# Kernel optimization log

Hardware: AMD Instinct MI355X
Metric: run time of the kernel (lower is better)

Reference implementation:

```python
import jax, jax.numpy as jnp
import numpy as np

# ---- static config (from MACEConfig / MACELayerConfig) ----
N_NODES = 128
F_S = 128          # n_invariant_feat_hidden (0e channels)
F_V = 64           # n_vectors_hidden (1e channels)
N_BESSEL = 8       # bessel_number
R_MAX = 5.0        # r_max
N_LAYERS = 2       # n_interactions
HID_RAD = 64       # radial MLP hidden width
F_S_OUT = 128      # n_invariant_feat_readout
F_V_OUT = 64       # n_vectors_readout
AVG_NEIGH = float(N_NODES)  # avg_num_neighbors default = n_nodes
RAD_OUT = F_S + 3 * F_V     # per-edge radial channel weights for the 4 TP paths


def _senders_receivers(n):
    # fully connected graph, matching get_senders_and_receivers
    s = np.repeat(np.arange(n), n - 1)
    j = np.tile(np.arange(1, n), n)
    r = (s + j) % n
    return jnp.asarray(s, dtype=jnp.int32), jnp.asarray(r, dtype=jnp.int32)


def _bessel(r):
    # e3nn bessel basis: sqrt(2/c) sin(n pi r / c) / r, n = 1..N_BESSEL
    n = jnp.arange(1, N_BESSEL + 1, dtype=r.dtype)
    return jnp.sqrt(2.0 / R_MAX) * jnp.sin(n * jnp.pi * r[:, None] / R_MAX) / r[:, None]


def _envelope(r):
    # smooth radial cutoff (polynomial p=6), stand-in for e3nn soft_envelope
    u = r / R_MAX
    p = 6.0
    env = 1.0 - (p + 1) * (p + 2) / 2 * u ** p + p * (p + 2) * u ** (p + 1) - p * (p + 1) / 2 * u ** (p + 2)
    return jnp.where(u < 1.0, env, 0.0)


def _forward(x, species_embed, Wr1, Wr2, W_sv, W_mix_s, W_mix_v, W_out_s, W_out_v):
    senders, receivers = _senders_receivers(N_NODES)

    def single(pos):  # pos: (N, 3)
        com = pos.mean(axis=0)                       # centre of mass (3,)
        v = pos[receivers] - pos[senders]            # edge relative vectors (E, 3)
        r = jnp.linalg.norm(v, axis=-1) + 1e-8       # (E,)
        vhat = v / r[:, None]
        rb = _bessel(r) * _envelope(r)[:, None]      # (E, N_BESSEL)

        s = jnp.broadcast_to(species_embed[0], (N_NODES, F_S))       # 0e node feats
        V = jnp.zeros((N_NODES, F_V, 3), dtype=pos.dtype)            # 1e node feats

        for l in range(N_LAYERS):
            # learned per-edge radial weights for each tensor-product path
            h = jax.nn.silu(rb @ Wr1[l]) @ Wr2[l]    # (E, RAD_OUT)
            R0 = h[:, :F_S]
            R1 = h[:, F_S:F_S + F_V]
            R2 = h[:, F_S + F_V:F_S + 2 * F_V]
            R3 = h[:, F_S + 2 * F_V:]

            s_src = s[senders]                       # gather (E, F_S)
            V_src = V[senders]                       # gather (E, F_V, 3)

            # CG tensor-product paths (only 0e and 1e irreps present):
            m0a = R0 * s_src                                         # 0e x 0e -> 0e
            m0b = R1 * jnp.einsum('efk,ek->ef', V_src, vhat)         # 1e x 1e -> 0e
            m1a = (R2 * (s_src @ W_sv[l]))[..., None] * vhat[:, None, :]  # 0e x 1e -> 1e
            m1b = R3[..., None] * V_src                              # 1e x 0e -> 1e

            # scatter-sum message passing over receivers
            agg0 = jax.ops.segment_sum(jnp.concatenate([m0a, m0b], -1), receivers,
                                       num_segments=N_NODES) / AVG_NEIGH   # (N, F_S+F_V)
            agg1 = jax.ops.segment_sum(jnp.concatenate([m1a, m1b], 1), receivers,
                                       num_segments=N_NODES) / AVG_NEIGH   # (N, 2F_V, 3)

            s = s + jax.nn.silu(agg0 @ W_mix_s[l])
            V = V + jnp.einsum('nfk,fg->ngk', agg1, W_mix_v[l])

        out_s = s @ W_out_s                                          # (N, F_S_OUT)
        out_v = jnp.einsum('nfk,fg->ngk', V, W_out_v) + com          # (N, F_V_OUT, 3) + CoM
        return out_v, out_s

    return jax.vmap(single)(x)


def setup_inputs() -> dict:
    key = jax.random.key(0)
    ks = jax.random.split(key, 10)
    sc = lambda fan: 1.0 / np.sqrt(fan)
    inp = {
        'x': jax.random.normal(ks[0], (8, N_NODES, 3), dtype=jnp.float32),
        'species_embed': jax.random.normal(ks[1], (1, F_S), dtype=jnp.float32),
        'Wr1': jax.random.normal(ks[2], (N_LAYERS, N_BESSEL, HID_RAD), dtype=jnp.float32) * sc(N_BESSEL),
        'Wr2': jax.random.normal(ks[3], (N_LAYERS, HID_RAD, RAD_OUT), dtype=jnp.float32) * sc(HID_RAD),
        'W_sv': jax.random.normal(ks[4], (N_LAYERS, F_S, F_V), dtype=jnp.float32) * sc(F_S),
        'W_mix_s': jax.random.normal(ks[5], (N_LAYERS, F_S + F_V, F_S), dtype=jnp.float32) * sc(F_S + F_V),
        'W_mix_v': jax.random.normal(ks[6], (N_LAYERS, 2 * F_V, F_V), dtype=jnp.float32) * sc(2 * F_V),
        'W_out_s': jax.random.normal(ks[7], (F_S, F_S_OUT), dtype=jnp.float32) * sc(F_S),
        'W_out_v': jax.random.normal(ks[8], (F_V, F_V_OUT), dtype=jnp.float32) * sc(F_V),
    }
    return inp


def reference(x, species_embed, Wr1, Wr2, W_sv, W_mix_s, W_mix_v, W_out_s, W_out_v):
    return _forward(x, species_embed, Wr1, Wr2, W_sv, W_mix_s, W_mix_v, W_out_s, W_out_v)
```

## Files before the change

### kernel.cpp

```cpp
#include <hip/hip_runtime.h>
#include <math.h>

typedef unsigned short u16;
typedef __attribute__((ext_vector_type(8))) short frag_ab;
typedef __attribute__((ext_vector_type(4))) float frag_cd;

#define BATCH 8
#define NN 128
#define FS 128
#define FV 64
#define NB 8
#define HID 64
#define ROUT 320
#define HSTRB 72

#define SZ_S (BATCH*FS*NN)
#define SZ_V (BATCH*FV*3*NN)
#define SZ_T (BATCH*FV*NN)
#define N_W2B (ROUT*HID)
#define OFF_SB 0
#define OFF_VB (OFF_SB+SZ_S)
#define OFF_T1 (OFF_VB+SZ_V)
#define OFF_W2B (OFF_T1+SZ_T)

__device__ __forceinline__ float silu_f(float x){ return x * (1.0f/(1.0f + __expf(-x))); }

__device__ __forceinline__ u16 f2bf(float x){
  union { float f; unsigned int u; } v; v.f = x;
  unsigned int r = v.u + 0x7fffu + ((v.u >> 16) & 1u);
  return (u16)(r >> 16);
}
__device__ __forceinline__ float bf2f(u16 h){
  union { unsigned int u; float f; } v; v.u = ((unsigned int)h) << 16; return v.f;
}

__global__ __launch_bounds__(512) void layer0_kernel(
    const float* __restrict__ pos,
    const float* __restrict__ species,
    const float* __restrict__ Wr1l,
    const float* __restrict__ Wr2,
    const float* __restrict__ Wsv,
    const float* __restrict__ WmixSl,
    const float* __restrict__ WmixVl,
    float* __restrict__ sOut,
    float* __restrict__ vOut,
    float* __restrict__ tOut,
    u16*   __restrict__ w2b)
{
  const int tid = threadIdx.x;
  const int b   = blockIdx.x >> 6;
  const int k0  = (blockIdx.x & 63) * 2;

  __shared__ u16   hidB[2][128*HSTRB];
  __shared__ float vhx[2][128], vhy[2][128], vhz[2][128];
  __shared__ float colsum[2][4][64];
  __shared__ float aggS[2][128];
  __shared__ float dV[2][192];
  __shared__ float sNew[2][128];
  __shared__ float t0L[64];

  const float* pb   = pos + b*NN*3;
  const float* Wr2l = Wr2;

  {
    const int kk   = tid >> 8;
    const int r2   = tid & 255;
    const int i    = r2 & 127;
    const int half = r2 >> 7;
    const int k    = k0 + kk;
    float vx = pb[k*3+0]-pb[i*3+0];
    float vy = pb[k*3+1]-pb[i*3+1];
    float vz = pb[k*3+2]-pb[i*3+2];
    float r = sqrtf(vx*vx+vy*vy+vz*vz) + 1e-8f;
    float inv = 1.0f/r;
    if (half==0){ vhx[kk][i]=vx*inv; vhy[kk][i]=vy*inv; vhz[kk][i]=vz*inv; }
    float u = r*0.2f;
    float env = 0.0f;
    if (u < 1.0f && i != k){
      float u2=u*u, u6=u2*u2*u2;
      env = 1.0f - 28.0f*u6 + 48.0f*u6*u - 21.0f*u6*u2;
    }
    float coef = 0.6324555320336759f * inv * env;
    float th   = r * 0.6283185307179586f;
    float s1 = __sinf(th), c1 = __cosf(th);
    float rb[NB];
    rb[0] = coef*s1;
    float twoc = 2.f*c1, sp = s1, spp = 0.f;
    #pragma unroll
    for(int n=1;n<NB;n++){ float s = twoc*sp - spp; spp = sp; sp = s; rb[n] = coef*s; }
    u16* hrow = hidB[kk] + i*HSTRB;
    #pragma unroll
    for(int jg=0;jg<8;jg++){
      const int jgg = half*8 + jg;
      float h0=0.f,h1=0.f,h2=0.f,h3=0.f;
      #pragma unroll
      for(int n=0;n<NB;n++){
        const float* wr = Wr1l + n*HID + jgg*4;
        float rn = rb[n];
        h0 = fmaf(rn, wr[0], h0);
        h1 = fmaf(rn, wr[1], h1);
        h2 = fmaf(rn, wr[2], h2);
        h3 = fmaf(rn, wr[3], h3);
      }
      ushort4 uu = make_ushort4(f2bf(silu_f(h0)), f2bf(silu_f(h1)),
                                f2bf(silu_f(h2)), f2bf(silu_f(h3)));
      *(ushort4*)(hrow + jgg*4) = uu;
    }
  }
  __syncthreads();

  {
    const int kk  = tid >> 8;
    const int var = (tid >> 6) & 3;
    const int j   = tid & 63;
    const u16* hb = hidB[kk];
    float a0 = 0.f, a1 = 0.f;
    if (var == 0){
      #pragma unroll 8
      for (int i=0;i<128;i+=2){
        a0 += bf2f(hb[i*HSTRB + j]);
        a1 += bf2f(hb[(i+1)*HSTRB + j]);
      }
    } else {
      const float* wv = (var==1) ? vhx[kk] : (var==2) ? vhy[kk] : vhz[kk];
      #pragma unroll 8
      for (int i=0;i<128;i+=2){
        a0 = fmaf(bf2f(hb[i*HSTRB + j]),     wv[i],   a0);
        a1 = fmaf(bf2f(hb[(i+1)*HSTRB + j]), wv[i+1], a1);
      }
    }
    colsum[kk][var][j] = a0+a1;
  }
  __syncthreads();

  if (tid < 128){
    const int c = tid;
    float d00=0.f,d01=0.f, d10=0.f,d11=0.f;
    #pragma unroll 8
    for (int j=0;j<HID;j+=2){
      float w0 = Wr2l[j*ROUT + c];
      float w1 = Wr2l[(j+1)*ROUT + c];
      d00 = fmaf(colsum[0][0][j],   w0, d00);
      d01 = fmaf(colsum[0][0][j+1], w1, d01);
      d10 = fmaf(colsum[1][0][j],   w0, d10);
      d11 = fmaf(colsum[1][0][j+1], w1, d11);
    }
    float sc = species[c] * (1.0f/128.0f);
    aggS[0][c] = sc * (d00+d01);
    aggS[1][c] = sc * (d10+d11);
  } else if (tid < 320){
    const int o = tid - 128;
    const int f = o & 63, c3 = o >> 6;
    float d00=0.f,d01=0.f, d10=0.f,d11=0.f;
    #pragma unroll 8
    for (int j=0;j<HID;j+=2){
      float w0 = Wr2l[j*ROUT + 192 + f];
      float w1 = Wr2l[(j+1)*ROUT + 192 + f];
      d00 = fmaf(colsum[0][1+c3][j],   w0, d00);
      d01 = fmaf(colsum[0][1+c3][j+1], w1, d01);
      d10 = fmaf(colsum[1][1+c3][j],   w0, d10);
      d11 = fmaf(colsum[1][1+c3][j+1], w1, d11);
    }
    dV[0][f*3+c3] = (d00+d01) * (1.0f/128.0f);
    dV[1][f*3+c3] = (d10+d11) * (1.0f/128.0f);
  } else if (tid < 384){
    const int g = tid - 320;
    float a0=0.f, a1=0.f;
    #pragma unroll 8
    for (int c=0; c<FS; c+=2){
      a0 = fmaf(species[c],   Wsv[c*FV+g],     a0);
      a1 = fmaf(species[c+1], Wsv[(c+1)*FV+g], a1);
    }
    t0L[g] = a0+a1;
  } else if (tid < 424){
    const int t = blockIdx.x*40 + (tid-384);
    const int j = t & 63, c = t >> 6;
    w2b[t] = f2bf(Wr2[HID*ROUT + j*ROUT + c]);
  }
  __syncthreads();

  if (tid < FS){
    float a00=0.f,a01=0.f, a10=0.f,a11=0.f;
    #pragma unroll 8
    for (int cc=0; cc<128; cc+=2){
      float w0 = WmixSl[cc*FS+tid];
      float w1 = WmixSl[(cc+1)*FS+tid];
      a00 = fmaf(aggS[0][cc],   w0, a00);
      a01 = fmaf(aggS[0][cc+1], w1, a01);
      a10 = fmaf(aggS[1][cc],   w0, a10);
      a11 = fmaf(aggS[1][cc+1], w1, a11);
    }
    float sn0 = species[tid] + silu_f(a00+a01);
    float sn1 = species[tid] + silu_f(a10+a11);
    sNew[0][tid] = sn0;
    sNew[1][tid] = sn1;
    sOut[(b*FS+tid)*NN + k0]     = sn0;
    sOut[(b*FS+tid)*NN + k0 + 1] = sn1;
  } else if (tid < 320){
    const int o = tid - 128;
    const int g = o/3, c3 = o - g*3;
    float a0=0.f, a1=0.f;
    #pragma unroll 8
    for (int f=0; f<FV; f++){
      float w = WmixVl[f*FV+g];
      float tf = t0L[f];
      a0 = fmaf(tf*dV[0][f*3+c3], w, a0);
      a1 = fmaf(tf*dV[1][f*3+c3], w, a1);
    }
    vOut[(b*FV*3 + o)*NN + k0]     = a0;
    vOut[(b*FV*3 + o)*NN + k0 + 1] = a1;
  }
  __syncthreads();

  if (tid < FV){
    const float* Wsv1 = Wsv + FS*FV;
    float a00=0.f,a01=0.f, a10=0.f,a11=0.f;
    #pragma unroll 8
    for (int f=0; f<FS; f+=2){
      float w0 = Wsv1[f*FV+tid];
      float w1 = Wsv1[(f+1)*FV+tid];
      a00 = fmaf(sNew[0][f],   w0, a00);
      a01 = fmaf(sNew[0][f+1], w1, a01);
      a10 = fmaf(sNew[1][f],   w0, a10);
      a11 = fmaf(sNew[1][f+1], w1, a11);
    }
    tOut[(b*FV+tid)*NN + k0]     = (a00+a01);
    tOut[(b*FV+tid)*NN + k0 + 1] = (a10+a11);
  }
}

__global__ __launch_bounds__(512) void layer_kernel(
    const float* __restrict__ pos,
    const float* __restrict__ sIn,
    const float* __restrict__ vIn,
    const float* __restrict__ tIn,
    const float* __restrict__ Wr1l,
    const u16*   __restrict__ w2bl,
    const float* __restrict__ WmixSl,
    const float* __restrict__ WmixVl,
    const float* __restrict__ WoutS,
    const float* __restrict__ WoutV,
    float* __restrict__ outp)
{
  const int tid  = threadIdx.x;
  const int b    = blockIdx.x >> 5;
  const int k0   = (blockIdx.x & 31) * 4;
  const int w    = tid >> 6;
  const int lane = tid & 63;
  const int col  = lane & 15;
  const int quad = lane >> 4;
  const int wq   = w & 3;
  const int sh   = w >> 2;

  __shared__ u16   hidB[4][128*HSTRB];
  __shared__ float vhx[4][128], vhy[4][128], vhz[4][128];
  __shared__ float aggP[4][2][576];
  __shared__ float sPart[4][2][FS];
  __shared__ float sNew[4][FS];
  __shared__ float vNewL[4][192];
  __shared__ float comL[3];

  const float* pb = pos + b*NN*3;

  {
    const int kk = tid >> 7;
    const int i  = tid & 127;
    const int k  = k0 + kk;
    float vx = pb[k*3+0]-pb[i*3+0];
    float vy = pb[k*3+1]-pb[i*3+1];
    float vz = pb[k*3+2]-pb[i*3+2];
    float r = sqrtf(vx*vx+vy*vy+vz*vz) + 1e-8f;
    float inv = 1.0f/r;
    vhx[kk][i]=vx*inv; vhy[kk][i]=vy*inv; vhz[kk][i]=vz*inv;
    float u = r*0.2f;
    float env = 0.0f;
    if (u < 1.0f && i != k){
      float u2=u*u, u6=u2*u2*u2;
      env = 1.0f - 28.0f*u6 + 48.0f*u6*u - 21.0f*u6*u2;
    }
    float coef = 0.6324555320336759f * inv * env;
    float th   = r * 0.6283185307179586f;
    float s1 = __sinf(th), c1 = __cosf(th);
    float rb[NB];
    rb[0] = coef*s1;
    float twoc = 2.f*c1, sp = s1, spp = 0.f;
    #pragma unroll
    for(int n=1;n<NB;n++){ float s = twoc*sp - spp; spp = sp; sp = s; rb[n] = coef*s; }
    u16* hrow = hidB[kk] + i*HSTRB;
    #pragma unroll
    for(int jg=0;jg<16;jg++){
      float h0=0.f,h1=0.f,h2=0.f,h3=0.f;
      #pragma unroll
      for(int n=0;n<NB;n++){
        const float* wr = Wr1l + n*HID + jg*4;
        float rn = rb[n];
        h0 = fmaf(rn, wr[0], h0);
        h1 = fmaf(rn, wr[1], h1);
        h2 = fmaf(rn, wr[2], h2);
        h3 = fmaf(rn, wr[3], h3);
      }
      ushort4 uu = make_ushort4(f2bf(silu_f(h0)), f2bf(silu_f(h1)),
                                f2bf(silu_f(h2)), f2bf(silu_f(h3)));
      *(ushort4*)(hrow + jg*4) = uu;
    }
    if (tid < 3){
      float a0=0.f, a1=0.f;
      for (int n=0;n<NN;n+=2){ a0 += pb[n*3+tid]; a1 += pb[(n+1)*3+tid]; }
      comL[tid] = (a0+a1) * (1.0f/128.0f);
    }
  }
  __syncthreads();

  const float* sIb = sIn + b*FS*NN;
  const float* vIb = vIn + b*FV*3*NN;
  const float* tIb = tIn + b*FV*NN;
  const int i00 = sh*64 + quad*4;

  {
    const int c_s0 = wq*16 + col;
    const int c_s1 = 64 + c_s0;
    const int f_vc = c_s0;

    const u16* wp0 = w2bl + c_s0*HID + quad*8;
    const u16* wp1 = w2bl + c_s1*HID + quad*8;
    const u16* wp2 = w2bl + (128 + f_vc)*HID + quad*8;
    const u16* wp3 = w2bl + (192 + f_vc)*HID + quad*8;
    const u16* wp4 = w2bl + (256 + f_vc)*HID + quad*8;
    const frag_ab b00 = *(const frag_ab*)(wp0), b01 = *(const frag_ab*)(wp0+32);
    const frag_ab b10 = *(const frag_ab*)(wp1), b11 = *(const frag_ab*)(wp1+32);
    const frag_ab b20 = *(const frag_ab*)(wp2), b21 = *(const frag_ab*)(wp2+32);
    const frag_ab b30 = *(const frag_ab*)(wp3), b31 = *(const frag_ab*)(wp3+32);
    const frag_ab b40 = *(const frag_ab*)(wp4), b41 = *(const frag_ab*)(wp4+32);

    const float* fs0 = sIb + c_s0*NN + i00;
    const float* fs1 = sIb + c_s1*NN + i00;
    const float* fv  = vIb + f_vc*3*NN + i00;
    const float* ft  = tIb + f_vc*NN + i00;

    float sA0[4]={0.f,0.f,0.f,0.f}, sA1[4]={0.f,0.f,0.f,0.f}, sA2[4]={0.f,0.f,0.f,0.f};
    float sX3[4]={0.f,0.f,0.f,0.f}, sY3[4]={0.f,0.f,0.f,0.f}, sZ3[4]={0.f,0.f,0.f,0.f};
    float sX4[4]={0.f,0.f,0.f,0.f}, sY4[4]={0.f,0.f,0.f,0.f}, sZ4[4]={0.f,0.f,0.f,0.f};

    #pragma unroll 1
    for (int mt=0; mt<4; mt++){
      float4 s4a = *(const float4*)&fs0[mt*16];
      float4 s4b = *(const float4*)&fs1[mt*16];
      float4 vx4 = *(const float4*)&fv[mt*16];
      float4 vy4 = *(const float4*)&fv[NN + mt*16];
      float4 vz4 = *(const float4*)&fv[2*NN + mt*16];
      float4 t4  = *(const float4*)&ft[mt*16];
      const int hbase = (sh*64 + mt*16 + col)*HSTRB + quad*8;
      const int vbase = i00 + mt*16;
      #pragma unroll
      for (int kk=0; kk<4; kk++){
        frag_ab a0 = *(const frag_ab*)&hidB[kk][hbase];
        frag_ab a1 = *(const frag_ab*)&hidB[kk][hbase + 32];
        float4 hx4 = *(const float4*)&vhx[kk][vbase];
        float4 hy4 = *(const float4*)&vhy[kk][vbase];
        float4 hz4 = *(const float4*)&vhz[kk][vbase];
        frag_cd ac0 = {0.f,0.f,0.f,0.f};
        frag_cd ac1 = {0.f,0.f,0.f,0.f};
        frag_cd ac2 = {0.f,0.f,0.f,0.f};
        frag_cd ac3 = {0.f,0.f,0.f,0.f};
        frag_cd ac4 = {0.f,0.f,0.f,0.f};
        ac0 = __builtin_amdgcn_mfma_f32_16x16x32_bf16(a0, b00, ac0, 0,0,0);
        ac1 = __builtin_amdgcn_mfma_f32_16x16x32_bf16(a0, b10, ac1, 0,0,0);
        ac2 = __builtin_amdgcn_mfma_f32_16x16x32_bf16(a0, b20, ac2, 0,0,0);
        ac3 = __builtin_amdgcn_mfma_f32_16x16x32_bf16(a0, b30, ac3, 0,0,0);
        ac4 = __builtin_amdgcn_mfma_f32_16x16x32_bf16(a0, b40, ac4, 0,0,0);
        ac0 = __builtin_amdgcn_mfma_f32_16x16x32_bf16(a1, b01, ac0, 0,0,0);
        ac1 = __builtin_amdgcn_mfma_f32_16x16x32_bf16(a1, b11, ac1, 0,0,0);
        ac2 = __builtin_amdgcn_mfma_f32_16x16x32_bf16(a1, b21, ac2, 0,0,0);
        ac3 = __builtin_amdgcn_mfma_f32_16x16x32_bf16(a1, b31, ac3, 0,0,0);
        ac4 = __builtin_amdgcn_mfma_f32_16x16x32_bf16(a1, b41, ac4, 0,0,0);

        sA0[kk] += ac0[0]*s4a.x + ac0[1]*s4a.y + ac0[2]*s4a.z + ac0[3]*s4a.w;
        sA1[kk] += ac1[0]*s4b.x + ac1[1]*s4b.y + ac1[2]*s4b.z + ac1[3]*s4b.w;
        sA2[kk] += ac2[0]*(vx4.x*hx4.x + vy4.x*hy4.x + vz4.x*hz4.x)
                 + ac2[1]*(vx4.y*hx4.y + vy4.y*hy4.y + vz4.y*hz4.y)
                 + ac2[2]*(vx4.z*hx4.z + vy4.z*hy4.z + vz4.z*hz4.z)
                 + ac2[3]*(vx4.w*hx4.w + vy4.w*hy4.w + vz4.w*hz4.w);
        float t0_ = ac3[0]*t4.x, t1_ = ac3[1]*t4.y, t2_ = ac3[2]*t4.z, t3_ = ac3[3]*t4.w;
        sX3[kk] += t0_*hx4.x + t1_*hx4.y + t2_*hx4.z + t3_*hx4.w;
        sY3[kk] += t0_*hy4.x + t1_*hy4.y + t2_*hy4.z + t3_*hy4.w;
        sZ3[kk] += t0_*hz4.x + t1_*hz4.y + t2_*hz4.z + t3_*hz4.w;
        sX4[kk] += ac4[0]*vx4.x + ac4[1]*vx4.y + ac4[2]*vx4.z + ac4[3]*vx4.w;
        sY4[kk] += ac4[0]*vy4.x + ac4[1]*vy4.y + ac4[2]*vy4.z + ac4[3]*vy4.w;
        sZ4[kk] += ac4[0]*vz4.x + ac4[1]*vz4.y + ac4[2]*vz4.z + ac4[3]*vz4.w;
      }
    }

    #pragma unroll
    for (int kk=0; kk<4; kk++){
      float v0 = sA0[kk]; v0 += __shfl_xor(v0,16,64); v0 += __shfl_xor(v0,32,64);
      float v1 = sA1[kk]; v1 += __shfl_xor(v1,16,64); v1 += __shfl_xor(v1,32,64);
      float v2 = sA2[kk]; v2 += __shfl_xor(v2,16,64); v2 += __shfl_xor(v2,32,64);
      float x3 = sX3[kk]; x3 += __shfl_xor(x3,16,64); x3 += __shfl_xor(x3,32,64);
      float y3 = sY3[kk]; y3 += __shfl_xor(y3,16,64); y3 += __shfl_xor(y3,32,64);
      float z3 = sZ3[kk]; z3 += __shfl_xor(z3,16,64); z3 += __shfl_xor(z3,32,64);
      float x4 = sX4[kk]; x4 += __shfl_xor(x4,16,64); x4 += __shfl_xor(x4,32,64);
      float y4 = sY4[kk]; y4 += __shfl_xor(y4,16,64); y4 += __shfl_xor(y4,32,64);
      float z4 = sZ4[kk]; z4 += __shfl_xor(z4,16,64); z4 += __shfl_xor(z4,32,64);
      if (lane < 16){
        aggP[kk][sh][wq*16 + lane]        = v0;
        aggP[kk][sh][64 + wq*16 + lane]   = v1;
        aggP[kk][sh][128 + wq*16 + lane]  = v2;
        const int f2 = wq*16 + lane;
        aggP[kk][sh][192+f2*3+0] = x3; aggP[kk][sh][192+f2*3+1] = y3; aggP[kk][sh][192+f2*3+2] = z3;
        aggP[kk][sh][384+f2*3+0] = x4; aggP[kk][sh][384+f2*3+1] = y4; aggP[kk][sh][384+f2*3+2] = z4;
      }
    }
  }

  __syncthreads();
  for (int t2=tid; t2<2304; t2+=512){
    const int kk = t2 / 576;
    const int t  = t2 - kk*576;
    aggP[kk][0][t] = (aggP[kk][0][t] + aggP[kk][1][t]) * (1.0f/128.0f);
  }
  __syncthreads();

  if (tid < 256){
    const int o = tid & 127, p = tid >> 7;
    const int c0 = p*96;
    float a0=0.f,a1=0.f,a2=0.f,a3=0.f;
    #pragma unroll 8
    for (int cc=c0; cc<c0+96; cc++){
      float w0 = WmixSl[cc*FS+o];
      a0 = fmaf(aggP[0][0][cc], w0, a0);
      a1 = fmaf(aggP[1][0][cc], w0, a1);
      a2 = fmaf(aggP[2][0][cc], w0, a2);
      a3 = fmaf(aggP[3][0][cc], w0, a3);
    }
    sPart[0][p][o] = a0; sPart[1][p][o] = a1;
    sPart[2][p][o] = a2; sPart[3][p][o] = a3;
  } else if (tid < 448){
    const int o = tid - 256;
    const int g = o/3, c3 = o - g*3;
    float a0=0.f,a1=0.f,a2=0.f,a3=0.f;
    #pragma unroll 8
    for (int f=0; f<FV; f++){
      float w0 = WmixVl[f*FV+g];
      float w1 = WmixVl[(f+FV)*FV+g];
      a0 = fmaf(aggP[0][0][192+f*3+c3], w0, a0); a0 = fmaf(aggP[0][0][384+f*3+c3], w1, a0);
      a1 = fmaf(aggP[1][0][192+f*3+c3], w0, a1); a1 = fmaf(aggP[1][0][384+f*3+c3], w1, a1);
      a2 = fmaf(aggP[2][0][192+f*3+c3], w0, a2); a2 = fmaf(aggP[2][0][384+f*3+c3], w1, a2);
      a3 = fmaf(aggP[3][0][192+f*3+c3], w0, a3); a3 = fmaf(aggP[3][0][384+f*3+c3], w1, a3);
    }
    vNewL[0][o] = vIb[o*NN + k0]     + a0;
    vNewL[1][o] = vIb[o*NN + k0 + 1] + a1;
    vNewL[2][o] = vIb[o*NN + k0 + 2] + a2;
    vNewL[3][o] = vIb[o*NN + k0 + 3] + a3;
  }
  __syncthreads();

  if (tid < FS){
    #pragma unroll
    for (int kk=0; kk<4; kk++)
      sNew[kk][tid] = sIb[tid*NN + k0 + kk] + silu_f(sPart[kk][0][tid] + sPart[kk][1][tid]);
  } else if (tid < 320){
    const int o = tid - 128;
    const int g = o/3, c3 = o - g*3;
    float a0 = comL[c3], a1 = comL[c3], a2 = comL[c3], a3 = comL[c3];
    #pragma unroll 8
    for (int f=0; f<FV; f++){
      float wv = WoutV[f*FV+g];
      a0 = fmaf(vNewL[0][f*3+c3], wv, a0);
      a1 = fmaf(vNewL[1][f*3+c3], wv, a1);
      a2 = fmaf(vNewL[2][f*3+c3], wv, a2);
      a3 = fmaf(vNewL[3][f*3+c3], wv, a3);
    }
    outp[(b*NN+k0)*FV*3 + o]   = a0;
    outp[(b*NN+k0+1)*FV*3 + o] = a1;
    outp[(b*NN+k0+2)*FV*3 + o] = a2;
    outp[(b*NN+k0+3)*FV*3 + o] = a3;
  }
  __syncthreads();

  if (tid < FS){
    float a0=0.f,a1=0.f,a2=0.f,a3=0.f;
    #pragma unroll 8
    for (int f=0; f<FS; f++){
      float w0 = WoutS[f*FS+tid];
      a0 = fmaf(sNew[0][f], w0, a0);
      a1 = fmaf(sNew[1][f], w0, a1);
      a2 = fmaf(sNew[2][f], w0, a2);
      a3 = fmaf(sNew[3][f], w0, a3);
    }
    outp[BATCH*NN*FV*3 + (b*NN+k0)*FS + tid]   = a0;
    outp[BATCH*NN*FV*3 + (b*NN+k0+1)*FS + tid] = a1;
    outp[BATCH*NN*FV*3 + (b*NN+k0+2)*FS + tid] = a2;
    outp[BATCH*NN*FV*3 + (b*NN+k0+3)*FS + tid] = a3;
  }
}

extern "C" void kernel_launch(void* const* d_in, const int* in_sizes, int n_in,
                              void* d_out, int out_size, void* d_ws, size_t ws_size,
                              hipStream_t stream)
{
  const float* x       = (const float*)d_in[0];
  const float* species = (const float*)d_in[1];
  const float* Wr1     = (const float*)d_in[2];
  const float* Wr2     = (const float*)d_in[3];
  const float* Wsv     = (const float*)d_in[4];
  const float* WmixS   = (const float*)d_in[5];
  const float* WmixV   = (const float*)d_in[6];
  const float* WoutS   = (const float*)d_in[7];
  const float* WoutV   = (const float*)d_in[8];
  float* ws  = (float*)d_ws;
  float* out = (float*)d_out;

  float* sB  = ws + OFF_SB;
  float* vB  = ws + OFF_VB;
  float* t1  = ws + OFF_T1;
  u16*   w2b = (u16*)(ws + OFF_W2B);

  layer0_kernel<<<BATCH*NN/2, 512, 0, stream>>>(x, species, Wr1, Wr2, Wsv,
      WmixS, WmixV, sB, vB, t1, w2b);

  layer_kernel<<<BATCH*NN/4, 512, 0, stream>>>(x, sB, vB, t1,
      Wr1 + NB*HID, w2b, WmixS + 192*FS, WmixV + 128*FV,
      WoutS, WoutV, out);
}
```

Before: 127.3 us.

## Double layer kernel block to 1024 threads, splitting MFMA paths across wave groups

The second-layer kernel now runs 1024 threads per block. Waves are split into two groups: one handles the scalar and scalar-from-vector tensor-product paths, the other the two vector-output paths. This cuts per-wave MFMA work and register pressure. The radial hidden computation, the WmixS reduction and the WoutS output matvec are each split over more threads, with extra shared-memory partial sums. The trade-offs are an extra barrier and partial-sum pass, and possible occupancy limits from the 1024-thread launch bound.

```diff
diff --git a/kernel.cpp b/kernel.cpp
--- a/kernel.cpp
+++ b/kernel.cpp
@@ -229,7 +229,7 @@
   }
 }
 
-__global__ __launch_bounds__(512) void layer_kernel(
+__global__ __launch_bounds__(1024) void layer_kernel(
     const float* __restrict__ pos,
     const float* __restrict__ sIn,
     const float* __restrict__ vIn,
@@ -249,13 +249,14 @@
   const int lane = tid & 63;
   const int col  = lane & 15;
   const int quad = lane >> 4;
-  const int wq   = w & 3;
-  const int sh   = w >> 2;
+  const int gh   = w & 1;
+  const int wq   = (w >> 1) & 3;
+  const int sh   = w >> 3;
 
   __shared__ u16   hidB[4][128*HSTRB];
   __shared__ float vhx[4][128], vhy[4][128], vhz[4][128];
   __shared__ float aggP[4][2][576];
-  __shared__ float sPart[4][2][FS];
+  __shared__ float sPart[4][4][FS];
   __shared__ float sNew[4][FS];
   __shared__ float vNewL[4][192];
   __shared__ float comL[3];
@@ -263,7 +264,8 @@
   const float* pb = pos + b*NN*3;
 
   {
-    const int kk = tid >> 7;
+    const int jh = tid >> 9;
+    const int kk = (tid >> 7) & 3;
     const int i  = tid & 127;
     const int k  = k0 + kk;
     float vx = pb[k*3+0]-pb[i*3+0];
@@ -271,7 +273,7 @@
     float vz = pb[k*3+2]-pb[i*3+2];
     float r = sqrtf(vx*vx+vy*vy+vz*vz) + 1e-8f;
     float inv = 1.0f/r;
-    vhx[kk][i]=vx*inv; vhy[kk][i]=vy*inv; vhz[kk][i]=vz*inv;
+    if (jh == 0){ vhx[kk][i]=vx*inv; vhy[kk][i]=vy*inv; vhz[kk][i]=vz*inv; }
     float u = r*0.2f;
     float env = 0.0f;
     if (u < 1.0f && i != k){
@@ -288,7 +290,8 @@
     for(int n=1;n<NB;n++){ float s = twoc*sp - spp; spp = sp; sp = s; rb[n] = coef*s; }
     u16* hrow = hidB[kk] + i*HSTRB;
     #pragma unroll
-    for(int jg=0;jg<16;jg++){
+    for(int jg0=0;jg0<8;jg0++){
+      const int jg = jh*8 + jg0;
       float h0=0.f,h1=0.f,h2=0.f,h3=0.f;
       #pragma unroll
       for(int n=0;n<NB;n++){
@@ -316,35 +319,84 @@
   const float* tIb = tIn + b*FV*NN;
   const int i00 = sh*64 + quad*4;
 
-  {
+  if (gh == 0){
     const int c_s0 = wq*16 + col;
     const int c_s1 = 64 + c_s0;
-    const int f_vc = c_s0;
 
     const u16* wp0 = w2bl + c_s0*HID + quad*8;
     const u16* wp1 = w2bl + c_s1*HID + quad*8;
-    const u16* wp2 = w2bl + (128 + f_vc)*HID + quad*8;
-    const u16* wp3 = w2bl + (192 + f_vc)*HID + quad*8;
-    const u16* wp4 = w2bl + (256 + f_vc)*HID + quad*8;
+    const u16* wp2 = w2bl + (128 + c_s0)*HID + quad*8;
     const frag_ab b00 = *(const frag_ab*)(wp0), b01 = *(const frag_ab*)(wp0+32);
     const frag_ab b10 = *(const frag_ab*)(wp1), b11 = *(const frag_ab*)(wp1+32);
     const frag_ab b20 = *(const frag_ab*)(wp2), b21 = *(const frag_ab*)(wp2+32);
-    const frag_ab b30 = *(const frag_ab*)(wp3), b31 = *(const frag_ab*)(wp3+32);
-    const frag_ab b40 = *(const frag_ab*)(wp4), b41 = *(const frag_ab*)(wp4+32);
 
     const float* fs0 = sIb + c_s0*NN + i00;
     const float* fs1 = sIb + c_s1*NN + i00;
-    const float* fv  = vIb + f_vc*3*NN + i00;
-    const float* ft  = tIb + f_vc*NN + i00;
+    const float* fv  = vIb + c_s0*3*NN + i00;
 
     float sA0[4]={0.f,0.f,0.f,0.f}, sA1[4]={0.f,0.f,0.f,0.f}, sA2[4]={0.f,0.f,0.f,0.f};
-    float sX3[4]={0.f,0.f,0.f,0.f}, sY3[4]={0.f,0.f,0.f,0.f}, sZ3[4]={0.f,0.f,0.f,0.f};
-    float sX4[4]={0.f,0.f,0.f,0.f}, sY4[4]={0.f,0.f,0.f,0.f}, sZ4[4]={0.f,0.f,0.f,0.f};
 
     #pragma unroll 1
     for (int mt=0; mt<4; mt++){
       float4 s4a = *(const float4*)&fs0[mt*16];
       float4 s4b = *(const float4*)&fs1[mt*16];
+      float4 vx4 = *(const float4*)&fv[mt*16];
+      float4 vy4 = *(const float4*)&fv[NN + mt*16];
+      float4 vz4 = *(const float4*)&fv[2*NN + mt*16];
+      const int hbase = (sh*64 + mt*16 + col)*HSTRB + quad*8;
+      const int vbase = i00 + mt*16;
+      #pragma unroll
+      for (int kk=0; kk<4; kk++){
+        frag_ab a0 = *(const frag_ab*)&hidB[kk][hbase];
+        frag_ab a1 = *(const frag_ab*)&hidB[kk][hbase + 32];
+        float4 hx4 = *(const float4*)&vhx[kk][vbase];
+        float4 hy4 = *(const float4*)&vhy[kk][vbase];
+        float4 hz4 = *(const float4*)&vhz[kk][vbase];
+        frag_cd ac0 = {0.f,0.f,0.f,0.f};
+        frag_cd ac1 = {0.f,0.f,0.f,0.f};
+        frag_cd ac2 = {0.f,0.f,0.f,0.f};
+        ac0 = __builtin_amdgcn_mfma_f32_16x16x32_bf16(a0, b00, ac0, 0,0,0);
+        ac1 = __builtin_amdgcn_mfma_f32_16x16x32_bf16(a0, b10, ac1, 0,0,0);
+        ac2 = __builtin_amdgcn_mfma_f32_16x16x32_bf16(a0, b20, ac2, 0,0,0);
+        ac0 = __builtin_amdgcn_mfma_f32_16x16x32_bf16(a1, b01, ac0, 0,0,0);
+        ac1 = __builtin_amdgcn_mfma_f32_16x16x32_bf16(a1, b11, ac1, 0,0,0);
+        ac2 = __builtin_amdgcn_mfma_f32_16x16x32_bf16(a1, b21, ac2, 0,0,0);
+
+        sA0[kk] += ac0[0]*s4a.x + ac0[1]*s4a.y + ac0[2]*s4a.z + ac0[3]*s4a.w;
+        sA1[kk] += ac1[0]*s4b.x + ac1[1]*s4b.y + ac1[2]*s4b.z + ac1[3]*s4b.w;
+        sA2[kk] += ac2[0]*(vx4.x*hx4.x + vy4.x*hy4.x + vz4.x*hz4.x)
+                 + ac2[1]*(vx4.y*hx4.y + vy4.y*hy4.y + vz4.y*hz4.y)
+                 + ac2[2]*(vx4.z*hx4.z + vy4.z*hy4.z + vz4.z*hz4.z)
+                 + ac2[3]*(vx4.w*hx4.w + vy4.w*hy4.w + vz4.w*hz4.w);
+      }
+    }
+    #pragma unroll
+    for (int kk=0; kk<4; kk++){
+      float v0 = sA0[kk]; v0 += __shfl_xor(v0,16,64); v0 += __shfl_xor(v0,32,64);
+      float v1 = sA1[kk]; v1 += __shfl_xor(v1,16,64); v1 += __shfl_xor(v1,32,64);
+      float v2 = sA2[kk]; v2 += __shfl_xor(v2,16,64); v2 += __shfl_xor(v2,32,64);
+      if (lane < 16){
+        aggP[kk][sh][wq*16 + lane]       = v0;
+        aggP[kk][sh][64 + wq*16 + lane]  = v1;
+        aggP[kk][sh][128 + wq*16 + lane] = v2;
+      }
+    }
+  } else {
+    const int f_vc = wq*16 + col;
+
+    const u16* wp3 = w2bl + (192 + f_vc)*HID + quad*8;
+    const u16* wp4 = w2bl + (256 + f_vc)*HID + quad*8;
+    const frag_ab b30 = *(const frag_ab*)(wp3), b31 = *(const frag_ab*)(wp3+32);
+    const frag_ab b40 = *(const frag_ab*)(wp4), b41 = *(const frag_ab*)(wp4+32);
+
+    const float* fv = vIb + f_vc*3*NN + i00;
+    const float* ft = tIb + f_vc*NN + i00;
+
+    float sX3[4]={0.f,0.f,0.f,0.f}, sY3[4]={0.f,0.f,0.f,0.f}, sZ3[4]={0.f,0.f,0.f,0.f};
+    float sX4[4]={0.f,0.f,0.f,0.f}, sY4[4]={0.f,0.f,0.f,0.f}, sZ4[4]={0.f,0.f,0.f,0.f};
+
+    #pragma unroll 1
+    for (int mt=0; mt<4; mt++){
       float4 vx4 = *(const float4*)&fv[mt*16];
       float4 vy4 = *(const float4*)&fv[NN + mt*16];
       float4 vz4 = *(const float4*)&fv[2*NN + mt*16];
@@ -358,28 +410,13 @@
         float4 hx4 = *(const float4*)&vhx[kk][vbase];
         float4 hy4 = *(const float4*)&vhy[kk][vbase];
         float4 hz4 = *(const float4*)&vhz[kk][vbase];
-        frag_cd ac0 = {0.f,0.f,0.f,0.f};
-        frag_cd ac1 = {0.f,0.f,0.f,0.f};
-        frag_cd ac2 = {0.f,0.f,0.f,0.f};
         frag_cd ac3 = {0.f,0.f,0.f,0.f};
         frag_cd ac4 = {0.f,0.f,0.f,0.f};
-        ac0 = __builtin_amdgcn_mfma_f32_16x16x32_bf16(a0, b00, ac0, 0,0,0);
-        ac1 = __builtin_amdgcn_mfma_f32_16x16x32_bf16(a0, b10, ac1, 0,0,0);
-        ac2 = __builtin_amdgcn_mfma_f32_16x16x32_bf16(a0, b20, ac2, 0,0,0);
         ac3 = __builtin_amdgcn_mfma_f32_16x16x32_bf16(a0, b30, ac3, 0,0,0);
         ac4 = __builtin_amdgcn_mfma_f32_16x16x32_bf16(a0, b40, ac4, 0,0,0);
-        ac0 = __builtin_amdgcn_mfma_f32_16x16x32_bf16(a1, b01, ac0, 0,0,0);
-        ac1 = __builtin_amdgcn_mfma_f32_16x16x32_bf16(a1, b11, ac1, 0,0,0);
-        ac2 = __builtin_amdgcn_mfma_f32_16x16x32_bf16(a1, b21, ac2, 0,0,0);
         ac3 = __builtin_amdgcn_mfma_f32_16x16x32_bf16(a1, b31, ac3, 0,0,0);
         ac4 = __builtin_amdgcn_mfma_f32_16x16x32_bf16(a1, b41, ac4, 0,0,0);
 
-        sA0[kk] += ac0[0]*s4a.x + ac0[1]*s4a.y + ac0[2]*s4a.z + ac0[3]*s4a.w;
-        sA1[kk] += ac1[0]*s4b.x + ac1[1]*s4b.y + ac1[2]*s4b.z + ac1[3]*s4b.w;
-        sA2[kk] += ac2[0]*(vx4.x*hx4.x + vy4.x*hy4.x + vz4.x*hz4.x)
-                 + ac2[1]*(vx4.y*hx4.y + vy4.y*hy4.y + vz4.y*hz4.y)
-                 + ac2[2]*(vx4.z*hx4.z + vy4.z*hy4.z + vz4.z*hz4.z)
-                 + ac2[3]*(vx4.w*hx4.w + vy4.w*hy4.w + vz4.w*hz4.w);
         float t0_ = ac3[0]*t4.x, t1_ = ac3[1]*t4.y, t2_ = ac3[2]*t4.z, t3_ = ac3[3]*t4.w;
         sX3[kk] += t0_*hx4.x + t1_*hx4.y + t2_*hx4.z + t3_*hx4.w;
         sY3[kk] += t0_*hy4.x + t1_*hy4.y + t2_*hy4.z + t3_*hy4.w;
@@ -389,12 +426,8 @@
         sZ4[kk] += ac4[0]*vz4.x + ac4[1]*vz4.y + ac4[2]*vz4.z + ac4[3]*vz4.w;
       }
     }
-
     #pragma unroll
     for (int kk=0; kk<4; kk++){
-      float v0 = sA0[kk]; v0 += __shfl_xor(v0,16,64); v0 += __shfl_xor(v0,32,64);
-      float v1 = sA1[kk]; v1 += __shfl_xor(v1,16,64); v1 += __shfl_xor(v1,32,64);
-      float v2 = sA2[kk]; v2 += __shfl_xor(v2,16,64); v2 += __shfl_xor(v2,32,64);
       float x3 = sX3[kk]; x3 += __shfl_xor(x3,16,64); x3 += __shfl_xor(x3,32,64);
       float y3 = sY3[kk]; y3 += __shfl_xor(y3,16,64); y3 += __shfl_xor(y3,32,64);
       float z3 = sZ3[kk]; z3 += __shfl_xor(z3,16,64); z3 += __shfl_xor(z3,32,64);
@@ -402,9 +435,6 @@
       float y4 = sY4[kk]; y4 += __shfl_xor(y4,16,64); y4 += __shfl_xor(y4,32,64);
       float z4 = sZ4[kk]; z4 += __shfl_xor(z4,16,64); z4 += __shfl_xor(z4,32,64);
       if (lane < 16){
-        aggP[kk][sh][wq*16 + lane]        = v0;
-        aggP[kk][sh][64 + wq*16 + lane]   = v1;
-        aggP[kk][sh][128 + wq*16 + lane]  = v2;
         const int f2 = wq*16 + lane;
         aggP[kk][sh][192+f2*3+0] = x3; aggP[kk][sh][192+f2*3+1] = y3; aggP[kk][sh][192+f2*3+2] = z3;
         aggP[kk][sh][384+f2*3+0] = x4; aggP[kk][sh][384+f2*3+1] = y4; aggP[kk][sh][384+f2*3+2] = z4;
@@ -413,19 +443,19 @@
   }
 
   __syncthreads();
-  for (int t2=tid; t2<2304; t2+=512){
+  for (int t2=tid; t2<2304; t2+=1024){
     const int kk = t2 / 576;
     const int t  = t2 - kk*576;
     aggP[kk][0][t] = (aggP[kk][0][t] + aggP[kk][1][t]) * (1.0f/128.0f);
   }
   __syncthreads();
 
-  if (tid < 256){
+  if (tid < 512){
     const int o = tid & 127, p = tid >> 7;
-    const int c0 = p*96;
+    const int c0 = p*48;
     float a0=0.f,a1=0.f,a2=0.f,a3=0.f;
     #pragma unroll 8
-    for (int cc=c0; cc<c0+96; cc++){
+    for (int cc=c0; cc<c0+48; cc++){
       float w0 = WmixSl[cc*FS+o];
       a0 = fmaf(aggP[0][0][cc], w0, a0);
       a1 = fmaf(aggP[1][0][cc], w0, a1);
@@ -434,8 +464,8 @@
     }
     sPart[0][p][o] = a0; sPart[1][p][o] = a1;
     sPart[2][p][o] = a2; sPart[3][p][o] = a3;
-  } else if (tid < 448){
-    const int o = tid - 256;
+  } else if (tid < 704){
+    const int o = tid - 512;
     const int g = o/3, c3 = o - g*3;
     float a0=0.f,a1=0.f,a2=0.f,a3=0.f;
     #pragma unroll 8
@@ -457,7 +487,9 @@
   if (tid < FS){
     #pragma unroll
     for (int kk=0; kk<4; kk++)
-      sNew[kk][tid] = sIb[tid*NN + k0 + kk] + silu_f(sPart[kk][0][tid] + sPart[kk][1][tid]);
+      sNew[kk][tid] = sIb[tid*NN + k0 + kk]
+                    + silu_f(sPart[kk][0][tid] + sPart[kk][1][tid]
+                           + sPart[kk][2][tid] + sPart[kk][3][tid]);
   } else if (tid < 320){
     const int o = tid - 128;
     const int g = o/3, c3 = o - g*3;
@@ -477,20 +509,31 @@
   }
   __syncthreads();
 
-  if (tid < FS){
+  float* e3s = &aggP[0][0][0];
+  if (tid < 512){
+    const int o = tid & 127, p = tid >> 7;
+    const int f0 = p*32;
     float a0=0.f,a1=0.f,a2=0.f,a3=0.f;
     #pragma unroll 8
-    for (int f=0; f<FS; f++){
-      float w0 = WoutS[f*FS+tid];
+    for (int f=f0; f<f0+32; f++){
+      float w0 = WoutS[f*FS+o];
       a0 = fmaf(sNew[0][f], w0, a0);
       a1 = fmaf(sNew[1][f], w0, a1);
       a2 = fmaf(sNew[2][f], w0, a2);
       a3 = fmaf(sNew[3][f], w0, a3);
     }
-    outp[BATCH*NN*FV*3 + (b*NN+k0)*FS + tid]   = a0;
-    outp[BATCH*NN*FV*3 + (b*NN+k0+1)*FS + tid] = a1;
-    outp[BATCH*NN*FV*3 + (b*NN+k0+2)*FS + tid] = a2;
-    outp[BATCH*NN*FV*3 + (b*NN+k0+3)*FS + tid] = a3;
+    e3s[(p*4+0)*128 + o] = a0;
+    e3s[(p*4+1)*128 + o] = a1;
+    e3s[(p*4+2)*128 + o] = a2;
+    e3s[(p*4+3)*128 + o] = a3;
+  }
+  __syncthreads();
+
+  if (tid < 512){
+    const int o = tid & 127, kk = tid >> 7;
+    float a = e3s[(0*4+kk)*128 + o] + e3s[(1*4+kk)*128 + o]
+            + e3s[(2*4+kk)*128 + o] + e3s[(3*4+kk)*128 + o];
+    outp[BATCH*NN*FV*3 + (b*NN+k0+kk)*FS + o] = a;
   }
 }
 
@@ -518,7 +561,7 @@
   layer0_kernel<<<BATCH*NN/2, 512, 0, stream>>>(x, species, Wr1, Wr2, Wsv,
       WmixS, WmixV, sB, vB, t1, w2b);
 
-  layer_kernel<<<BATCH*NN/4, 512, 0, stream>>>(x, sB, vB, t1,
+  layer_kernel<<<BATCH*NN/4, 1024, 0, stream>>>(x, sB, vB, t1,
       Wr1 + NB*HID, w2b, WmixS + 192*FS, WmixV + 128*FV,
       WoutS, WoutV, out);
 }
```

Measured after the change: 126.0 us. No clear change (-1.1%).
